# Optimization experiments

Hardware: AMD Instinct MI355X
Metric: run time of the kernel (lower is better)

Reference implementation:

```python
import jax, jax.numpy as jnp
import numpy as np

IN_CH = 512; OUT_CH = 512; NOISE_SIZE = 512; K = 3; A = 0.2
B = 4; H = 32
_G = float(np.sqrt(2.0 / (1.0 + A * A)))                 # leaky_relu gain, a=0.2
CONV_SCALE = _G / float(np.sqrt(IN_CH * K * K))          # equal-lr kaiming scale (fan_in = in_ch*3*3)
MS_SCALE = float(np.sqrt(2.0 / (NOISE_SIZE + IN_CH)))    # equal-lr xavier scale on make_s linear
RGB_SCALE = _G * float(np.sqrt(2.0 / (OUT_CH + 3)))      # equal-lr xavier scale on 1x1 to_rgb


def upsample2x(x):
    # torch F.interpolate(scale_factor=2, mode='bilinear', align_corners=False)
    b, c, h, w = x.shape
    return jax.image.resize(x, (b, c, 2 * h, 2 * w), method='bilinear')


def mod_conv(x, style, weight, bias, ms_w, ms_b, w_scale, demodulate, pad):
    # style -> per-sample input-channel scales s: (B, Cin)
    s = style @ (ms_w.T * MS_SCALE) + ms_b
    Wmod = (weight * w_scale)[None] * s[:, None, :, None, None]   # (B, Cout, Cin, k, k)
    if demodulate:
        d = jax.lax.rsqrt(jnp.sum(Wmod * Wmod, axis=(2, 3, 4)) + 1e-8)
        Wmod = Wmod * d[:, :, None, None, None]
    conv1 = lambda xi, wi: jax.lax.conv_general_dilated(
        xi[None], wi, (1, 1), [(pad, pad), (pad, pad)],
        dimension_numbers=('NCHW', 'OIHW', 'NCHW'))[0]
    y = jax.vmap(conv1)(x, Wmod)                                   # per-sample weights == grouped conv
    return y + bias[None, :, None, None]


def lrelu(x):
    return jnp.where(x >= 0, x, A * x)


def setup_inputs() -> dict:
    key = jax.random.key(0)
    ks = jax.random.split(key, 19)
    r = lambda i, shape: jax.random.normal(ks[i], shape, dtype=jnp.float32)
    return {
        'maps': r(0, (B, IN_CH, H, H)),
        'w': r(1, (B, NOISE_SIZE)),
        'rgb': r(2, (B, 3, H, H)),
        'noise0': r(3, (B, 1, 2 * H, 2 * H)),
        'noise1': r(4, (B, 1, 2 * H, 2 * H)),
        'conv0_w': r(5, (OUT_CH, IN_CH, K, K)),
        'conv0_b': 0.1 * r(6, (OUT_CH,)),
        'ms0_w': r(7, (IN_CH, NOISE_SIZE)),
        'ms0_b': jnp.ones((IN_CH,), jnp.float32),
        'ns0': 0.1 * r(8, (OUT_CH,)),
        'conv1_w': r(9, (OUT_CH, OUT_CH, K, K)),
        'conv1_b': 0.1 * r(10, (OUT_CH,)),
        'ms1_w': r(11, (OUT_CH, NOISE_SIZE)),
        'ms1_b': jnp.ones((OUT_CH,), jnp.float32),
        'ns1': 0.1 * r(12, (OUT_CH,)),
        'rgb_w': r(13, (3, OUT_CH, 1, 1)),
        'rgb_b': 0.1 * r(14, (3,)),
        'msr_w': r(15, (OUT_CH, NOISE_SIZE)),
        'msr_b': jnp.ones((OUT_CH,), jnp.float32),
    }


def reference(maps, w, rgb, noise0, noise1,
              conv0_w, conv0_b, ms0_w, ms0_b, ns0,
              conv1_w, conv1_b, ms1_w, ms1_b, ns1,
              rgb_w, rgb_b, msr_w, msr_b):
    # upsample branch (upsample=True)
    rgb = upsample2x(rgb)
    maps = upsample2x(maps)
    # layer 0: modulated conv -> noise -> leaky relu
    h = mod_conv(maps, w, conv0_w, conv0_b, ms0_w, ms0_b, CONV_SCALE, True, 1)
    h = lrelu(h + ns0[None, :, None, None] * noise0)
    # layer 1
    h = mod_conv(h, w, conv1_w, conv1_b, ms1_w, ms1_b, CONV_SCALE, True, 1)
    h = lrelu(h + ns1[None, :, None, None] * noise1)
    # to_rgb: 1x1 modulated conv, no demodulation
    rgb_out = rgb + mod_conv(h, w, rgb_w, rgb_b, msr_w, msr_b, RGB_SCALE, False, 0)
    return (rgb_out, h)
```

## Files before the change

### kernel.cpp

```cpp
#include <hip/hip_runtime.h>
#include <stdint.h>


#define BATCH 4
#define CH 512
#define NPP 4356
#define HOUT_OFF 49152

static constexpr double G_GAIN = 1.3867504905630728;
static constexpr float CONV_SCALE_F = (float)(G_GAIN / 67.88225099390857);
static constexpr float MS_SCALE_F = 0.044194173824159216f;
static constexpr float RGB_SCALE_F = (float)(G_GAIN * 1.4142135623730951 / 22.693611435820433);

typedef __attribute__((ext_vector_type(8))) short short8;
typedef __attribute__((ext_vector_type(4))) float floatx4;

#define OFF_S0     256
#define OFF_S1     (OFF_S0 + 8192)
#define OFF_SR     (OFF_S1 + 8192)
#define OFF_D0     (OFF_SR + 8192)
#define OFF_D1     (OFF_D0 + 8192)
#define OFF_B0F    (OFF_D1 + 8192)
#define OFF_B1F    (OFF_B0F + 2048)
#define OFF_NS0F   (OFF_B1F + 2048)
#define OFF_NS1F   (OFF_NS0F + 2048)
#define OFF_WMODR  (OFF_NS1F + 2048)
#define OFF_N0F    (OFF_WMODR + 24576)
#define OFF_N1F    (OFF_N0F + 65536)
#define OFF_WT0    (OFF_N1F + 65536)
#define WT_BYTES   4718592
#define OFF_WT1    (OFF_WT0 + WT_BYTES)
#define OFF_XP0    (OFF_WT1 + WT_BYTES)
#define XP_BYTES   17842176
#define OFF_XP1    (OFF_XP0 + XP_BYTES)

__device__ __forceinline__ float bf2f(unsigned short u) {
  return __uint_as_float(((unsigned int)u) << 16);
}
__device__ __forceinline__ unsigned short f2bf(float f) {
  unsigned int x = __float_as_uint(f);
  unsigned int r = x + 0x7FFFu + ((x >> 16) & 1u);
  return (unsigned short)(r >> 16);
}
__device__ __forceinline__ float ldin(const void* p, long i, int bf) {
  if (bf) return bf2f(((const unsigned short*)p)[i]);
  return ((const float*)p)[i];
}
__device__ __forceinline__ int bfflag_of(const void* msb) {
  return ((const unsigned int*)msb)[0] == 0x3F803F80u ? 1 : 0;
}
__device__ __forceinline__ void async_ld16(const void* g, void* l) {
  __builtin_amdgcn_global_load_lds(
      (const __attribute__((address_space(1))) unsigned int*)g,
      (__attribute__((address_space(3))) unsigned int*)l, 16, 0, 0);
}
__device__ __forceinline__ void upw(int o, int n_in, int& lo, int& hi, float& wlo) {
  int k = o >> 1;
  if (o & 1) { lo = k; hi = k + 1; if (hi > n_in - 1) hi = n_in - 1; wlo = 0.75f; }
  else       { lo = k - 1; if (lo < 0) lo = 0; hi = k; wlo = 0.25f; }
}

__global__ void k_pre(const void* w, const void* msw0, const void* msb0,
                      const void* msw1, const void* msb1,
                      const void* mswr, const void* msbr,
                      const void* b0, const void* b1, const void* nv0,
                      const void* nv1, const void* noise0, const void* noise1,
                      float* s0, float* s1, float* sr,
                      float* ob0, float* ob1, float* ons0, float* ons1,
                      float* on0, float* on1, unsigned short* Xp) {
  const int bf = bfflag_of(msb0);
  const int bid = blockIdx.x;
  if (bid < 264) {
    const int idx = bid * 256 + threadIdx.x;
    const int plane = idx / 132;
    const int rem = idx - plane * 132;
    const int row65 = rem >= 66;
    const int col = rem - (row65 ? 66 : 0);
    const short8 z = {0, 0, 0, 0, 0, 0, 0, 0};
    *(short8*)&Xp[((long)plane * NPP + (row65 ? 65 : 0) * 66 + col) * 8] = z;
    return;
  }
  if (bid < 648) {
    const int b2 = bid - 264;
    const int mat = b2 >> 7, chunk = b2 & 127;
    const int wv = threadIdx.x >> 6, lane = threadIdx.x & 63;
    const int i = chunk * 4 + wv;
    const void* msw; const void* msb; float* out;
    if (mat == 0)      { msw = msw0; msb = msb0; out = s0; }
    else if (mat == 1) { msw = msw1; msb = msb1; out = s1; }
    else               { msw = mswr; msb = msbr; out = sr; }
    float a[4] = {0.f, 0.f, 0.f, 0.f};
    const int n0 = lane * 8;
    if (bf) {
      short8 m8 = *(const short8*)((const unsigned short*)msw + (long)i * 512 + n0);
      for (int b = 0; b < 4; ++b) {
        short8 w8 = *(const short8*)((const unsigned short*)w + b * 512 + n0);
        float s = 0.f;
        for (int e = 0; e < 8; ++e)
          s += bf2f((unsigned short)m8[e]) * bf2f((unsigned short)w8[e]);
        a[b] = s;
      }
    } else {
      const float* mrow = (const float*)msw + (long)i * 512 + n0;
      float4 m0v = *(const float4*)mrow, m1v = *(const float4*)(mrow + 4);
      for (int b = 0; b < 4; ++b) {
        const float* wr = (const float*)w + b * 512 + n0;
        float4 w0v = *(const float4*)wr, w1v = *(const float4*)(wr + 4);
        a[b] = m0v.x * w0v.x + m0v.y * w0v.y + m0v.z * w0v.z + m0v.w * w0v.w +
               m1v.x * w1v.x + m1v.y * w1v.y + m1v.z * w1v.z + m1v.w * w1v.w;
      }
    }
    for (int off = 1; off < 64; off <<= 1)
      for (int b = 0; b < 4; ++b) a[b] += __shfl_xor(a[b], off, 64);
    if (lane == 0) {
      const float mb = ldin(msb, i, bf);
      for (int b = 0; b < 4; ++b) out[b * 512 + i] = a[b] * MS_SCALE_F + mb;
    }
    return;
  }
  const int t = (bid - 648) * 256 + threadIdx.x;
  if (t < 512) {
    ob0[t] = ldin(b0, t, bf); ob1[t] = ldin(b1, t, bf);
    ons0[t] = ldin(nv0, t, bf); ons1[t] = ldin(nv1, t, bf);
  }
  on0[t] = ldin(noise0, t, bf);
  on1[t] = ldin(noise1, t, bf);
}

__global__ void k_mid(const void* w0, const void* w1,
                      const float* s0, const float* s1, const float* sr,
                      const void* rw, unsigned short* Wt0, unsigned short* Wt1,
                      float* S0, float* S1, float* owmr,
                      const void* maps, unsigned short* Xp0, const void* msb) {
  const int bf = bfflag_of(msb);
  const int bid = blockIdx.x;
  __shared__ float smem[32 * 4 * 32];
  if (bid < 256) {
    const int l = bid >> 7, cog = bid & 127;
    const void* w = l ? w1 : w0;
    const float* s = l ? s1 : s0;
    unsigned short* Wt = l ? Wt1 : Wt0;
    float* S = l ? S1 : S0;
    const int co_sub = threadIdx.x >> 6;
    const int kb = (threadIdx.x >> 2) & 15, q = threadIdx.x & 3;
    const int co = cog * 4 + co_sub;
    const int ci0 = kb * 32 + q * 8;
    const long base = ((long)co * 512 + ci0) * 9;
    float v[9][8];
    if (bf) {
      const unsigned short* wp = (const unsigned short*)w + base;
      short8 r[9];
#pragma unroll
      for (int k = 0; k < 9; ++k) r[k] = *(const short8*)(wp + k * 8);
#pragma unroll
      for (int j = 0; j < 8; ++j)
#pragma unroll
        for (int t = 0; t < 9; ++t) {
          const int off = j * 9 + t;
          v[t][j] = bf2f((unsigned short)r[off >> 3][off & 7]);
        }
    } else {
      const float* wp = (const float*)w + base;
      float4 r[18];
#pragma unroll
      for (int k = 0; k < 18; ++k) r[k] = *(const float4*)(wp + k * 4);
#pragma unroll
      for (int j = 0; j < 8; ++j)
#pragma unroll
        for (int t = 0; t < 9; ++t) {
          const int off = j * 9 + t;
          const float4 rr = r[off >> 2];
          const int c2 = off & 3;
          v[t][j] = c2 == 0 ? rr.x : (c2 == 1 ? rr.y : (c2 == 2 ? rr.z : rr.w));
        }
    }
#pragma unroll
    for (int t = 0; t < 9; ++t) {
      short8 pk;
#pragma unroll
      for (int j = 0; j < 8; ++j) pk[j] = (short)f2bf(v[t][j]);
      *(short8*)&Wt[((long)(t * 16 + kb) * 4 + q) * 4096 + co * 8] = pk;
    }
    float wsq[8];
#pragma unroll
    for (int j = 0; j < 8; ++j) {
      float a = 0.f;
#pragma unroll
      for (int t = 0; t < 9; ++t) a += v[t][j] * v[t][j];
      wsq[j] = a;
    }
    float part[4];
#pragma unroll
    for (int b4 = 0; b4 < 4; ++b4) {
      const float* sp = s + b4 * 512 + ci0;
      float4 sa = *(const float4*)sp, sb = *(const float4*)(sp + 4);
      part[b4] = sa.x * sa.x * wsq[0] + sa.y * sa.y * wsq[1] +
                 sa.z * sa.z * wsq[2] + sa.w * sa.w * wsq[3] +
                 sb.x * sb.x * wsq[4] + sb.y * sb.y * wsq[5] +
                 sb.z * sb.z * wsq[6] + sb.w * sb.w * wsq[7];
    }
    for (int off = 1; off < 64; off <<= 1)
#pragma unroll
      for (int b4 = 0; b4 < 4; ++b4)
        part[b4] += __shfl_xor(part[b4], off, 64);
    if ((threadIdx.x & 63) == 0)
#pragma unroll
      for (int b4 = 0; b4 < 4; ++b4) S[b4 * 512 + co] = part[b4];
    return;
  }
  if (bid < 1280) {
    const int bid2 = bid - 256;
    const int t = bid2 & 15, kb = (bid2 >> 4) & 15, b = bid2 >> 8;
    float (*lds)[4][32] = (float(*)[4][32])smem;
    {
      const int ciq = threadIdx.x >> 5;
      const int x = threadIdx.x & 31;
      for (int cc = 0; cc < 4; ++cc) {
        const int ci = cc * 8 + ciq;
        const long cbase = ((long)(b * 512 + kb * 32 + ci)) << 10;
        for (int r = 0; r < 4; ++r) {
          int ir = 2 * t - 1 + r;
          ir = ir < 0 ? 0 : (ir > 31 ? 31 : ir);
          lds[ci][r][x] = ldin(maps, cbase + ir * 32 + x, bf);
        }
      }
    }
    __syncthreads();
    const int q = threadIdx.x >> 6, px = threadIdx.x & 63;
    int xlo, xhi; float wx;
    upw(px, 32, xlo, xhi, wx);
    float sv[8];
    for (int jj = 0; jj < 8; ++jj) sv[jj] = s0[b * 512 + kb * 32 + q * 8 + jj];
    for (int y = 0; y < 4; ++y) {
      const int yg = 4 * t + y;
      int ylo, yhi; float wy;
      upw(yg, 32, ylo, yhi, wy);
      const int rlo = ylo - (2 * t - 1), rhi = yhi - (2 * t - 1);
      short8 pk;
      for (int jj = 0; jj < 8; ++jj) {
        const int ci = q * 8 + jj;
        float vlo = wx * lds[ci][rlo][xlo] + (1.f - wx) * lds[ci][rlo][xhi];
        float vhi = wx * lds[ci][rhi][xlo] + (1.f - wx) * lds[ci][rhi][xhi];
        float v = (wy * vlo + (1.f - wy) * vhi) * sv[jj];
        pk[jj] = (short)f2bf(v);
      }
      *(short8*)&Xp0[((((long)b * 16 + kb) * 4 + q) * NPP + (yg + 1) * 66 + (px + 1)) * 8] = pk;
    }
    return;
  }
  const int i = (bid - 1280) * 256 + threadIdx.x;
  const int b = i / 1536; const int r = i - b * 1536;
  const int c = r >> 9; const int ci = r & 511;
  owmr[i] = RGB_SCALE_F * ldin(rw, c * 512 + ci, bf) * sr[b * 512 + ci];
}

#define MFMA16 __builtin_amdgcn_mfma_f32_16x16x32_bf16
template <int LAYER>
__global__ __launch_bounds__(256, 2) void k_conv(
    const unsigned short* __restrict__ Wt,
    const unsigned short* Xp,
    const float* __restrict__ Ssum,
    const float* __restrict__ bias,
    const float* __restrict__ nsc,
    const float* __restrict__ noise,
    const float* __restrict__ snext,
    unsigned short* XpOut,
    void* dout,
    const void* __restrict__ msb) {
  __shared__ __align__(16) unsigned short AB[32768];
  const int idx = blockIdx.x;
  const int mt = idx & 3, b = (idx >> 2) & 3, nt = idx >> 4;
  const int m0 = mt << 7, y0 = nt << 1;
  const int lane = threadIdx.x & 63, wv = threadIdx.x >> 6;
  const int wm = wv >> 1, wn = wv & 1;
  const int q = lane >> 4, l15 = lane & 15;

  const floatx4 vz = {0.f, 0.f, 0.f, 0.f};
  floatx4 c00 = vz, c01 = vz, c02 = vz, c03 = vz;
  floatx4 c10 = vz, c11 = vz, c12 = vz, c13 = vz;
  floatx4 c20 = vz, c21 = vz, c22 = vz, c23 = vz;
  floatx4 c30 = vz, c31 = vz, c32 = vz, c33 = vz;

  const int vA = (q << 10) + (wm << 9) + (l15 << 3);
  const int BB = 24576;
  const int vB   = BB + (q << 9) + (l15 << 3);
  const int vBm1 = BB + (q << 9) + ((l15 == 0 ? 0 : l15 - 1) << 3);
  const int vBp1 = BB + (q << 9) + ((l15 == 15 ? 15 : l15 + 1) << 3);
  const bool e0 = (l15 == 0), e15 = (l15 == 15);
  const int c6 = wv * 6;

  auto issueB2 = [&](int kb, int r0) {
    for (int r = 0; r < 2; ++r) {
      const int row = r0 + r;
      const unsigned short* src =
          Xp + ((((long)b * 16 + kb) * 4 + wv) * NPP + (long)(y0 + row) * 66 + 1 + lane) * 8;
      async_ld16(src, &AB[BB + ((row * 4 + wv) << 9)]);
    }
  };
  auto issueA = [&](int kb, int ky, int par) {
#pragma unroll
    for (int k = 0; k < 6; ++k) {
      const int c = c6 + k;
      const int half = c & 1, chunk = c >> 1;
      const int kx = chunk >> 2, qq = chunk & 3;
      const unsigned short* src =
          Wt + ((long)(((ky * 3 + kx) * 16 + kb) * 4 + qq) << 12) +
          ((m0 + half * 64 + lane) << 3);
      async_ld16(src, &AB[par * 12288 + chunk * 1024 + half * 512]);
    }
  };

  const short8 z8 = {0, 0, 0, 0, 0, 0, 0, 0};

#define RND(KY, PA, KB, NKB, NKY, NPA, DOB, DKB, DR0)                          \
  {                                                                            \
    __syncthreads();                                                           \
    issueA((NKB), (NKY), (NPA));                                               \
    if (DOB) issueB2((DKB), (DR0));                                            \
    const int ab = (PA) * 12288 + vA;                                          \
    short8 a00 = *(const short8*)&AB[ab];                                      \
    short8 a01 = *(const short8*)&AB[ab + 128];                                \
    short8 a02 = *(const short8*)&AB[ab + 256];                                \
    short8 a03 = *(const short8*)&AB[ab + 384];                                \
    short8 a10 = *(const short8*)&AB[ab + 4096];                               \
    short8 a11 = *(const short8*)&AB[ab + 4224];                               \
    short8 a12 = *(const short8*)&AB[ab + 4352];                               \
    short8 a13 = *(const short8*)&AB[ab + 4480];                               \
    short8 a20 = *(const short8*)&AB[ab + 8192];                               \
    short8 a21 = *(const short8*)&AB[ab + 8320];                               \
    short8 a22 = *(const short8*)&AB[ab + 8448];                               \
    short8 a23 = *(const short8*)&AB[ab + 8576];                               \
    const int bo = ((wn + (KY)) << 11);                                        \
    {                                                              \
      short8 b0 = *(const short8*)&AB[vBm1 + bo];                              \
      short8 b1 = *(const short8*)&AB[vB + bo + 120];                          \
      short8 b2 = *(const short8*)&AB[vB + bo + 248];                          \
      short8 b3 = *(const short8*)&AB[vB + bo + 376];                          \
      b0 = e0 ? z8 : b0;                                                       \
      c00 = MFMA16(a00, b0, c00, 0, 0, 0); c01 = MFMA16(a00, b1, c01, 0, 0, 0);\
      c02 = MFMA16(a00, b2, c02, 0, 0, 0); c03 = MFMA16(a00, b3, c03, 0, 0, 0);\
      c10 = MFMA16(a01, b0, c10, 0, 0, 0); c11 = MFMA16(a01, b1, c11, 0, 0, 0);\
      c12 = MFMA16(a01, b2, c12, 0, 0, 0); c13 = MFMA16(a01, b3, c13, 0, 0, 0);\
      c20 = MFMA16(a02, b0, c20, 0, 0, 0); c21 = MFMA16(a02, b1, c21, 0, 0, 0);\
      c22 = MFMA16(a02, b2, c22, 0, 0, 0); c23 = MFMA16(a02, b3, c23, 0, 0, 0);\
      c30 = MFMA16(a03, b0, c30, 0, 0, 0); c31 = MFMA16(a03, b1, c31, 0, 0, 0);\
      c32 = MFMA16(a03, b2, c32, 0, 0, 0); c33 = MFMA16(a03, b3, c33, 0, 0, 0);\
    }                                                                          \
    {                                                              \
      short8 b0 = *(const short8*)&AB[vB + bo];                                \
      short8 b1 = *(const short8*)&AB[vB + bo + 128];                          \
      short8 b2 = *(const short8*)&AB[vB + bo + 256];                          \
      short8 b3 = *(const short8*)&AB[vB + bo + 384];                          \
      c00 = MFMA16(a10, b0, c00, 0, 0, 0); c01 = MFMA16(a10, b1, c01, 0, 0, 0);\
      c02 = MFMA16(a10, b2, c02, 0, 0, 0); c03 = MFMA16(a10, b3, c03, 0, 0, 0);\
      c10 = MFMA16(a11, b0, c10, 0, 0, 0); c11 = MFMA16(a11, b1, c11, 0, 0, 0);\
      c12 = MFMA16(a11, b2, c12, 0, 0, 0); c13 = MFMA16(a11, b3, c13, 0, 0, 0);\
      c20 = MFMA16(a12, b0, c20, 0, 0, 0); c21 = MFMA16(a12, b1, c21, 0, 0, 0);\
      c22 = MFMA16(a12, b2, c22, 0, 0, 0); c23 = MFMA16(a12, b3, c23, 0, 0, 0);\
      c30 = MFMA16(a13, b0, c30, 0, 0, 0); c31 = MFMA16(a13, b1, c31, 0, 0, 0);\
      c32 = MFMA16(a13, b2, c32, 0, 0, 0); c33 = MFMA16(a13, b3, c33, 0, 0, 0);\
    }                                                                          \
    {                                                              \
      short8 b0 = *(const short8*)&AB[vB + bo + 8];                            \
      short8 b1 = *(const short8*)&AB[vB + bo + 136];                          \
      short8 b2 = *(const short8*)&AB[vB + bo + 264];                          \
      short8 b3 = *(const short8*)&AB[vBp1 + bo + 384];                        \
      b3 = e15 ? z8 : b3;                                                      \
      c00 = MFMA16(a20, b0, c00, 0, 0, 0); c01 = MFMA16(a20, b1, c01, 0, 0, 0);\
      c02 = MFMA16(a20, b2, c02, 0, 0, 0); c03 = MFMA16(a20, b3, c03, 0, 0, 0);\
      c10 = MFMA16(a21, b0, c10, 0, 0, 0); c11 = MFMA16(a21, b1, c11, 0, 0, 0);\
      c12 = MFMA16(a21, b2, c12, 0, 0, 0); c13 = MFMA16(a21, b3, c13, 0, 0, 0);\
      c20 = MFMA16(a22, b0, c20, 0, 0, 0); c21 = MFMA16(a22, b1, c21, 0, 0, 0);\
      c22 = MFMA16(a22, b2, c22, 0, 0, 0); c23 = MFMA16(a22, b3, c23, 0, 0, 0);\
      c30 = MFMA16(a23, b0, c30, 0, 0, 0); c31 = MFMA16(a23, b1, c31, 0, 0, 0);\
      c32 = MFMA16(a23, b2, c32, 0, 0, 0); c33 = MFMA16(a23, b3, c33, 0, 0, 0);\
    }                                                                          \
  }

  issueA(0, 0, 0);
  issueB2(0, 0);

#pragma unroll 1
  for (int it = 0; it < 8; ++it) {
    const int kb = it * 2, kb1 = kb + 1, kb2 = (kb + 2) & 15;
    RND(0, 0, kb,  kb,  1, 1, 1, kb,  2)
    RND(1, 1, kb,  kb,  2, 0, 0, 0,  0)
    RND(2, 0, kb,  kb1, 0, 1, 1, kb1, 0)
    RND(0, 1, kb1, kb1, 1, 0, 1, kb1, 2)
    RND(1, 0, kb1, kb1, 2, 1, 0, 0,  0)
    RND(2, 1, kb1, kb2, 0, 0, 1, kb2, 0)
  }
#undef RND

  floatx4 accv[4][4] = {{c00, c01, c02, c03}, {c10, c11, c12, c13},
                        {c20, c21, c22, c23}, {c30, c31, c32, c33}};
  const int bfflag = bfflag_of(msb);
  const int coB = m0 + (wm << 6) + ((lane >> 4) << 2);
  const int xB = lane & 15;
  const int y = y0 + wn;
  for (int i = 0; i < 4; ++i) {
    const int co = coB + (i << 4);
    float Ds[4], bi[4], nv[4], sx[4];
    for (int r = 0; r < 4; ++r) {
      float Sv = Ssum[b * 512 + co + r];
      Ds[r] = CONV_SCALE_F * rsqrtf(CONV_SCALE_F * CONV_SCALE_F * Sv + 1e-8f);
      bi[r] = bias[co + r];
      nv[r] = nsc[co + r];
      sx[r] = (LAYER == 0) ? snext[b * 512 + co + r] : 0.f;
    }
    for (int j = 0; j < 4; ++j) {
      const int x = (j << 4) + xB;
      const int p = (y << 6) + x;
      const float nz = noise[b * 4096 + p];
      if (LAYER == 0) {
        unsigned long long pk = 0ull;
        for (int r = 0; r < 4; ++r) {
          float v = accv[i][j][r] * Ds[r] + bi[r] + nv[r] * nz;
          v = (v >= 0.f) ? v : 0.2f * v;
          pk |= (unsigned long long)f2bf(v * sx[r]) << (16 * r);
        }
        const int pp = (y + 1) * 66 + (x + 1);
        const long o = ((((long)b * 16 + (co >> 5)) * 4 + ((co >> 3) & 3)) * NPP + pp) * 8 + (co & 7);
        *(unsigned long long*)(XpOut + o) = pk;
      } else {
        for (int r = 0; r < 4; ++r) {
          float v = accv[i][j][r] * Ds[r] + bi[r] + nv[r] * nz;
          v = (v >= 0.f) ? v : 0.2f * v;
          const long o = (((long)(b * 512 + co + r)) << 12) + p;
          if (bfflag) ((unsigned short*)dout)[HOUT_OFF + o] = f2bf(v);
          else        ((float*)dout)[HOUT_OFF + o] = v;
        }
      }
    }
  }
}

__global__ void k_rgb(const void* rgb_in, const float* wmodr, const void* rb,
                      void* dout, const void* msb) {
  const int bf = bfflag_of(msb);
  const int b = blockIdx.y, p0 = blockIdx.x * 512;
  const int g = threadIdx.x >> 6, lane = threadIdx.x & 63;
  const int px = p0 + lane * 8;
  const char* hbytes = (const char*)dout + (long)HOUT_OFF * (bf ? 2 : 4);
  const float* wm = wmodr + b * 1536;
  float a0[8] = {}, a1[8] = {}, a2[8] = {};
  for (int ci = g * 128; ci < g * 128 + 128; ++ci) {
    const long o = (((long)(b * 512 + ci)) << 12) + px;
    float hv[8];
    if (bf) {
      short8 h8 = *(const short8*)((const unsigned short*)hbytes + o);
#pragma unroll
      for (int k = 0; k < 8; ++k) hv[k] = bf2f((unsigned short)h8[k]);
    } else {
      float4 f0 = *(const float4*)((const float*)hbytes + o);
      float4 f1 = *(const float4*)((const float*)hbytes + o + 4);
      hv[0] = f0.x; hv[1] = f0.y; hv[2] = f0.z; hv[3] = f0.w;
      hv[4] = f1.x; hv[5] = f1.y; hv[6] = f1.z; hv[7] = f1.w;
    }
    const float w0 = wm[ci], w1 = wm[512 + ci], w2 = wm[1024 + ci];
#pragma unroll
    for (int k = 0; k < 8; ++k) {
      a0[k] += w0 * hv[k]; a1[k] += w1 * hv[k]; a2[k] += w2 * hv[k];
    }
  }
  __shared__ float red[4][3][512];
#pragma unroll
  for (int k = 0; k < 8; ++k) {
    red[g][0][lane * 8 + k] = a0[k];
    red[g][1][lane * 8 + k] = a1[k];
    red[g][2][lane * 8 + k] = a2[k];
  }
  __syncthreads();
  for (int e = 0; e < 2; ++e) {
    const int pp = threadIdx.x * 2 + e;
    const int p = p0 + pp;
    const int y = p >> 6, x = p & 63;
    int ylo, yhi, xlo, xhi; float wy, wx;
    upw(y, 32, ylo, yhi, wy);
    upw(x, 32, xlo, xhi, wx);
    for (int c = 0; c < 3; ++c) {
      float s = red[0][c][pp] + red[1][c][pp] + red[2][c][pp] + red[3][c][pp];
      const long base = (long)(b * 3 + c) << 10;
      const float v00 = ldin(rgb_in, base + ylo * 32 + xlo, bf);
      const float v01 = ldin(rgb_in, base + ylo * 32 + xhi, bf);
      const float v10 = ldin(rgb_in, base + yhi * 32 + xlo, bf);
      const float v11 = ldin(rgb_in, base + yhi * 32 + xhi, bf);
      const float up = wy * (wx * v00 + (1.f - wx) * v01) +
                       (1.f - wy) * (wx * v10 + (1.f - wx) * v11);
      const float v = up + s + ldin(rb, c, bf);
      const long o = ((long)(b * 3 + c) << 12) + p;
      if (bf) ((unsigned short*)dout)[o] = f2bf(v);
      else    ((float*)dout)[o] = v;
    }
  }
}

extern "C" void kernel_launch(void* const* d_in, const int* in_sizes, int n_in,
                              void* d_out, int out_size, void* d_ws, size_t ws_size,
                              hipStream_t stream) {
  char* ws = (char*)d_ws;
  float* s0 = (float*)(ws + OFF_S0);
  float* s1 = (float*)(ws + OFF_S1);
  float* sr = (float*)(ws + OFF_SR);
  float* S0 = (float*)(ws + OFF_D0);
  float* S1 = (float*)(ws + OFF_D1);
  float* b0f = (float*)(ws + OFF_B0F);
  float* b1f = (float*)(ws + OFF_B1F);
  float* ns0f = (float*)(ws + OFF_NS0F);
  float* ns1f = (float*)(ws + OFF_NS1F);
  float* wmodr = (float*)(ws + OFF_WMODR);
  float* n0f = (float*)(ws + OFF_N0F);
  float* n1f = (float*)(ws + OFF_N1F);
  unsigned short* Wt0 = (unsigned short*)(ws + OFF_WT0);
  unsigned short* Wt1 = (unsigned short*)(ws + OFF_WT1);
  unsigned short* Xp0 = (unsigned short*)(ws + OFF_XP0);
  unsigned short* Xp1 = (unsigned short*)(ws + OFF_XP1);

  k_pre<<<712, 256, 0, stream>>>(d_in[1], d_in[7], d_in[8], d_in[12], d_in[13],
                                 d_in[17], d_in[18], d_in[6], d_in[11], d_in[9],
                                 d_in[14], d_in[3], d_in[4],
                                 s0, s1, sr, b0f, b1f, ns0f, ns1f, n0f, n1f, Xp0);
  k_mid<<<1304, 256, 0, stream>>>(d_in[5], d_in[10], s0, s1, sr, d_in[15],
                                  Wt0, Wt1, S0, S1, wmodr, d_in[0], Xp0, d_in[8]);
  k_conv<0><<<512, 256, 0, stream>>>(Wt0, Xp0, S0, b0f, ns0f, n0f, s1, Xp1,
                                     d_out, d_in[8]);
  k_conv<1><<<512, 256, 0, stream>>>(Wt1, Xp1, S1, b1f, ns1f, n1f, s1, Xp1,
                                     d_out, d_in[8]);
  k_rgb<<<dim3(8, 4), 256, 0, stream>>>(d_in[2], wmodr, d_in[16], d_out, d_in[8]);
  (void)in_sizes; (void)n_in; (void)out_size; (void)ws_size;
}
```

Before: 293.7 us.

## Double conv block tile to 8 waves covering four output rows

Each conv block now has 512 threads (8 waves) and covers 128 output channels by four rows instead of two. The modulated-weight tile in LDS is shared by twice as many output pixels, which halves the weight traffic per output. The input rows are loaded as a six-row halo slab, double-buffered by channel block. In exchange the grid shrinks to 256 blocks and LDS per block grows to 96KB, which lowers occupancy and may leave CUs idle.

```diff
diff --git a/kernel.cpp b/kernel.cpp
--- a/kernel.cpp
+++ b/kernel.cpp
@@ -256,7 +256,7 @@
 
 #define MFMA16 __builtin_amdgcn_mfma_f32_16x16x32_bf16
 template <int LAYER>
-__global__ __launch_bounds__(256, 2) void k_conv(
+__global__ __launch_bounds__(512, 2) void k_conv(
     const unsigned short* __restrict__ Wt,
     const unsigned short* Xp,
     const float* __restrict__ Ssum,
@@ -267,12 +267,12 @@
     unsigned short* XpOut,
     void* dout,
     const void* __restrict__ msb) {
-  __shared__ __align__(16) unsigned short AB[32768];
+  __shared__ __align__(16) unsigned short AB[49152];
   const int idx = blockIdx.x;
   const int mt = idx & 3, b = (idx >> 2) & 3, nt = idx >> 4;
-  const int m0 = mt << 7, y0 = nt << 1;
+  const int m0 = mt << 7, y0 = nt << 2;
   const int lane = threadIdx.x & 63, wv = threadIdx.x >> 6;
-  const int wm = wv >> 1, wn = wv & 1;
+  const int wm = wv >> 2, wn = wv & 3;
   const int q = lane >> 4, l15 = lane & 15;
 
   const floatx4 vz = {0.f, 0.f, 0.f, 0.f};
@@ -283,40 +283,41 @@
 
   const int vA = (q << 10) + (wm << 9) + (l15 << 3);
   const int BB = 24576;
-  const int vB   = BB + (q << 9) + (l15 << 3);
-  const int vBm1 = BB + (q << 9) + ((l15 == 0 ? 0 : l15 - 1) << 3);
-  const int vBp1 = BB + (q << 9) + ((l15 == 15 ? 15 : l15 + 1) << 3);
+  const int vB   = (q << 9) + (l15 << 3);
+  const int vBm1 = (q << 9) + ((l15 == 0 ? 0 : l15 - 1) << 3);
+  const int vBp1 = (q << 9) + ((l15 == 15 ? 15 : l15 + 1) << 3);
   const bool e0 = (l15 == 0), e15 = (l15 == 15);
-  const int c6 = wv * 6;
-
-  auto issueB2 = [&](int kb, int r0) {
-    for (int r = 0; r < 2; ++r) {
-      const int row = r0 + r;
+
+  auto issueB6 = [&](int kbn, int half) {
+#pragma unroll
+    for (int k = 0; k < 3; ++k) {
+      const int t = wv * 3 + k;
+      const int row = t >> 2, qq = t & 3;
       const unsigned short* src =
-          Xp + ((((long)b * 16 + kb) * 4 + wv) * NPP + (long)(y0 + row) * 66 + 1 + lane) * 8;
-      async_ld16(src, &AB[BB + ((row * 4 + wv) << 9)]);
+          Xp + ((((long)b * 16 + kbn) * 4 + qq) * NPP + (long)(y0 + row) * 66 + 1 + lane) * 8;
+      async_ld16(src, &AB[BB + half * 12288 + ((row * 4 + qq) << 9)]);
     }
   };
   auto issueA = [&](int kb, int ky, int par) {
 #pragma unroll
-    for (int k = 0; k < 6; ++k) {
-      const int c = c6 + k;
-      const int half = c & 1, chunk = c >> 1;
+    for (int k = 0; k < 3; ++k) {
+      const int c = wv * 3 + k;
+      const int half64 = c & 1, chunk = c >> 1;
       const int kx = chunk >> 2, qq = chunk & 3;
       const unsigned short* src =
           Wt + ((long)(((ky * 3 + kx) * 16 + kb) * 4 + qq) << 12) +
-          ((m0 + half * 64 + lane) << 3);
-      async_ld16(src, &AB[par * 12288 + chunk * 1024 + half * 512]);
+          ((m0 + half64 * 64 + lane) << 3);
+      async_ld16(src, &AB[par * 12288 + chunk * 1024 + half64 * 512]);
     }
   };
 
   const short8 z8 = {0, 0, 0, 0, 0, 0, 0, 0};
 
-#define RND(KY, PA, KB, NKB, NKY, NPA, DOB, DKB, DR0)                          \
+#define RND(KY, PA, HB, KB, NKB, NKY, NPA, DOB, DKB, DHB)                      \
   {                                                                            \
     __syncthreads();                                                           \
     issueA((NKB), (NKY), (NPA));                                               \
-    if (DOB) issueB2((DKB), (DR0));                                            \
+    if (DOB) issueB6((DKB), (DHB));                                            \
     const int ab = (PA) * 12288 + vA;                                          \
     short8 a00 = *(const short8*)&AB[ab];                                      \
     short8 a01 = *(const short8*)&AB[ab + 128];                                \
@@ -330,7 +331,7 @@
     short8 a21 = *(const short8*)&AB[ab + 8320];                               \
     short8 a22 = *(const short8*)&AB[ab + 8448];                               \
     short8 a23 = *(const short8*)&AB[ab + 8576];                               \
-    const int bo = ((wn + (KY)) << 11);                                        \
+    const int bo = BB + (HB) * 12288 + ((wn + (KY)) << 11);                    \
     {                                                              \
       short8 b0 = *(const short8*)&AB[vBm1 + bo];                              \
       short8 b1 = *(const short8*)&AB[vB + bo + 120];                          \
@@ -378,17 +379,17 @@
   }
 
   issueA(0, 0, 0);
-  issueB2(0, 0);
+  issueB6(0, 0);
 
 #pragma unroll 1
   for (int it = 0; it < 8; ++it) {
     const int kb = it * 2, kb1 = kb + 1, kb2 = (kb + 2) & 15;
-    RND(0, 0, kb,  kb,  1, 1, 1, kb,  2)
-    RND(1, 1, kb,  kb,  2, 0, 0, 0,  0)
-    RND(2, 0, kb,  kb1, 0, 1, 1, kb1, 0)
-    RND(0, 1, kb1, kb1, 1, 0, 1, kb1, 2)
-    RND(1, 0, kb1, kb1, 2, 1, 0, 0,  0)
-    RND(2, 1, kb1, kb2, 0, 0, 1, kb2, 0)
+    RND(0, 0, 0, kb,  kb,  1, 1, 1, kb1, 1)
+    RND(1, 1, 0, kb,  kb,  2, 0, 0, 0,  0)
+    RND(2, 0, 0, kb,  kb1, 0, 1, 0, 0,  0)
+    RND(0, 1, 1, kb1, kb1, 1, 0, 1, kb2, 0)
+    RND(1, 0, 1, kb1, kb1, 2, 1, 0, 0,  0)
+    RND(2, 1, 1, kb1, kb2, 0, 0, 0, 0,  0)
   }
 #undef RND
 
@@ -522,9 +523,9 @@
                                  s0, s1, sr, b0f, b1f, ns0f, ns1f, n0f, n1f, Xp0);
   k_mid<<<1304, 256, 0, stream>>>(d_in[5], d_in[10], s0, s1, sr, d_in[15],
                                   Wt0, Wt1, S0, S1, wmodr, d_in[0], Xp0, d_in[8]);
-  k_conv<0><<<512, 256, 0, stream>>>(Wt0, Xp0, S0, b0f, ns0f, n0f, s1, Xp1,
+  k_conv<0><<<256, 512, 0, stream>>>(Wt0, Xp0, S0, b0f, ns0f, n0f, s1, Xp1,
                                      d_out, d_in[8]);
-  k_conv<1><<<512, 256, 0, stream>>>(Wt1, Xp1, S1, b1f, ns1f, n1f, s1, Xp1,
+  k_conv<1><<<256, 512, 0, stream>>>(Wt1, Xp1, S1, b1f, ns1f, n1f, s1, Xp1,
                                      d_out, d_in[8]);
   k_rgb<<<dim3(8, 4), 256, 0, stream>>>(d_in[2], wmodr, d_in[16], d_out, d_in[8]);
   (void)in_sizes; (void)n_in; (void)out_size; (void)ws_size;
```

Result: faster. 283.7 us (-3.4%).
